# Kernel optimization log

Measured on AMD Instinct MI355X. Metric: run time of the kernel, lower is better.

Reference implementation:

```python
import jax, jax.numpy as jnp
import numpy as np

SEQ, BATCH = 2048, 32
ENC_HS, DEC_HS = 512, 1024

def setup_inputs() -> dict:
    key = jax.random.key(0)
    k1, k2, k3, k4, k5 = jax.random.split(key, 5)
    return {
        "hidden": jax.random.normal(k1, (BATCH, DEC_HS), dtype=jnp.float32),
        "encoder_outputs": jax.random.normal(k2, (SEQ, BATCH, 2 * ENC_HS), dtype=jnp.float32),
        "attn_w": jax.random.normal(k3, (2 * ENC_HS + DEC_HS, DEC_HS), dtype=jnp.float32) * 0.02,
        "attn_b": jax.random.normal(k4, (DEC_HS,), dtype=jnp.float32) * 0.02,
        "v": jax.random.normal(k5, (DEC_HS,), dtype=jnp.float32),
    }

def reference(hidden, encoder_outputs, attn_w, attn_b, v):
    # encoder_outputs: [S, B, 2*enc_hs] -> [B, S, 2*enc_hs]
    enc = jnp.transpose(encoder_outputs, (1, 0, 2))
    B, S, _ = enc.shape
    # hidden: [B, dec_hs] broadcast to [B, S, dec_hs]
    h = jnp.broadcast_to(hidden[:, None, :], (B, S, hidden.shape[-1]))
    cat = jnp.concatenate([h, enc], axis=2)            # [B, S, 2*enc_hs+dec_hs]
    energy = jnp.tanh(cat @ attn_w + attn_b)            # [B, S, dec_hs]
    scores = jnp.einsum("bsd,d->bs", energy, v)        # [B, S]
    return jax.nn.softmax(scores, axis=1)
```

## Files before the change

kernel.cpp:

```cpp
#include <hip/hip_runtime.h>


typedef _Float16 f16;
typedef _Float16 half8 __attribute__((ext_vector_type(8)));
typedef float f32x4 __attribute__((ext_vector_type(4)));

#define KDIM 1024
#define SEQ  2048
#define MROWS 65536

typedef __attribute__((address_space(1))) void gvoid;
typedef __attribute__((address_space(3))) void svoid;

__device__ __forceinline__ void gload_lds16(const void* g, void* l) {
    __builtin_amdgcn_global_load_lds((const gvoid*)g, (svoid*)l, 16, 0, 0);
}

__global__ __launch_bounds__(256) void prep_w(const float* __restrict__ w,
                                              f16* __restrict__ wt) {
    int idx  = blockIdx.x * 256 + threadIdx.x;
    int kblk = idx & 3;
    int nloc = (idx >> 2) & 255;
    int tile = idx >> 10;
    int nq   = tile >> 5, ks = tile & 31;
    int n_g  = nq * 256 + nloc;
    int kbase = 1024 + ks * 32 + kblk * 8;
    half8 h;
#pragma unroll
    for (int j = 0; j < 8; ++j)
        h[j] = (f16)w[(size_t)(kbase + j) * 1024 + n_g];
    int p = nloc * 4 + ((kblk + (nloc >> 1)) & 3);
    *(half8*)&wt[(size_t)tile * 8192 + p * 8] = h;
}

__global__ __launch_bounds__(256) void prep_hb(const float* __restrict__ hidden,
                                               const float* __restrict__ attn_w,
                                               const float* __restrict__ attn_b,
                                               float* __restrict__ hb) {
    int b = blockIdx.x >> 2;
    int n = (blockIdx.x & 3) * 256 + threadIdx.x;
    const float* h = hidden + (size_t)b * 1024;
    float acc = attn_b[n];
#pragma unroll 8
    for (int k = 0; k < 1024; ++k)
        acc += h[k] * attn_w[(size_t)k * 1024 + n];
    hb[(size_t)b * 1024 + n] = acc;
}

__global__ __launch_bounds__(512, 2)
void fused_energy(const float* __restrict__ enc, const f16* __restrict__ wt,
                  const float* __restrict__ hb, const float* __restrict__ vvec,
                  float* __restrict__ partout) {
    __shared__ f16 Ws[4][8192];
    __shared__ f16 As[4][8192];
    __shared__ float red[4][256];

    const int tid  = threadIdx.x;
    const int lane = tid & 63;
    const int wv   = tid >> 6;
    const int wm   = wv >> 2;
    const int wn   = wv & 3;
    const int l15  = lane & 15;
    const int l4   = lane >> 4;

    const int bid   = blockIdx.x;
    const int xcd   = bid & 7;
    const int chunk = bid >> 3;
    const int mt    = xcd * 32 + (chunk >> 2);
    const int nq    = chunk & 3;
    const int mrow0 = mt * 256;
    const int ncol0 = nq * 256;

    const char* wtNq = (const char*)wt + (size_t)nq * 32 * 16384;

    const int ar  = tid >> 1;
    const int akp = tid & 1;
    const float* aG = enc + (size_t)(mrow0 + ar) * KDIM + akp * 16;
    const int kb0 = akp * 2;
    const int p0  = ar * 4 + ((kb0 + (ar >> 1)) & 3);
    const int p1  = ar * 4 + ((kb0 + 1 + (ar >> 1)) & 3);

    const int wOff = wv * 2048 + lane * 16;

    char* const WsB = (char*)&Ws[0][0];
    char* const AsB = (char*)&As[0][0];

    int aOffB[8], bOffB[4];
#pragma unroll
    for (int mi = 0; mi < 8; ++mi) {
        int r = wm * 128 + mi * 16 + l15;
        aOffB[mi] = (r * 4 + ((l4 + (r >> 1)) & 3)) * 16;
    }
#pragma unroll
    for (int nj = 0; nj < 4; ++nj) {
        int n = wn * 64 + nj * 16 + l15;
        bOffB[nj] = (n * 4 + ((l4 + (n >> 1)) & 3)) * 16;
    }

    const f32x4 zero = {0.f, 0.f, 0.f, 0.f};
    f32x4 acc[8][4];
#pragma unroll
    for (int mi = 0; mi < 8; ++mi)
#pragma unroll
        for (int nj = 0; nj < 4; ++nj) acc[mi][nj] = zero;

    f32x4 aE[4], aO[4];

#define STAGE_W(TT)                                                          \
    {                                                                        \
        const char* ws_ = wtNq + (size_t)(TT) * 16384 + wOff;                \
        char* wd_ = WsB + ((TT) & 3) * 16384 + wOff;                         \
        gload_lds16(ws_, wd_);                                               \
        gload_lds16(ws_ + 1024, wd_ + 1024);                                 \
    }
#define LOAD_A(TT, R)                                                        \
    {                                                                        \
        const float* p_ = aG + (TT) * 32;                                    \
        R[0] = *(const f32x4*)(p_);     R[1] = *(const f32x4*)(p_ + 4);      \
        R[2] = *(const f32x4*)(p_ + 8); R[3] = *(const f32x4*)(p_ + 12);     \
    }
#define WRITE_A(TT, R)                                                       \
    {                                                                        \
        half8 h0_, h1_;                                                      \
        _Pragma("unroll") for (int j = 0; j < 4; ++j) {                      \
            h0_[j] = (f16)R[0][j]; h0_[4 + j] = (f16)R[1][j];                \
            h1_[j] = (f16)R[2][j]; h1_[4 + j] = (f16)R[3][j];                \
        }                                                                    \
        char* ab_ = AsB + ((TT) & 3) * 16384;                                \
        *(half8*)(ab_ + p0 * 16) = h0_;                                      \
        *(half8*)(ab_ + p1 * 16) = h1_;                                      \
    }
#define COMPUTE(TT)                                                          \
    {                                                                        \
        const char* wb_ = WsB + ((TT) & 3) * 16384;                          \
        const char* ab_ = AsB + ((TT) & 3) * 16384;                          \
        half8 bf_[4];                                                        \
        _Pragma("unroll") for (int nj = 0; nj < 4; ++nj)                     \
            bf_[nj] = *(const half8*)(wb_ + bOffB[nj]);                      \
        __builtin_amdgcn_s_setprio(1);                                       \
        _Pragma("unroll") for (int mi = 0; mi < 8; ++mi) {                   \
            half8 af_ = *(const half8*)(ab_ + aOffB[mi]);                    \
            _Pragma("unroll") for (int nj = 0; nj < 4; ++nj)                 \
                acc[mi][nj] = __builtin_amdgcn_mfma_f32_16x16x32_f16(        \
                    af_, bf_[nj], acc[mi][nj], 0, 0, 0);                     \
        }                                                                    \
        __builtin_amdgcn_s_setprio(0);                                       \
    }

    STAGE_W(0); LOAD_A(0, aE);
    STAGE_W(1); LOAD_A(1, aO);
    asm volatile("s_waitcnt vmcnt(6)" ::: "memory");
    WRITE_A(0, aE);
    asm volatile("s_waitcnt lgkmcnt(0)" ::: "memory");
    __builtin_amdgcn_s_barrier();

    for (int t = 0; t < 30; t += 2) {
        STAGE_W(t + 2); LOAD_A(t + 2, aE);
        asm volatile("s_waitcnt vmcnt(6)" ::: "memory");
        WRITE_A(t + 1, aO);
        COMPUTE(t);
        asm volatile("s_waitcnt lgkmcnt(0)" ::: "memory");
        __builtin_amdgcn_s_barrier();

        STAGE_W(t + 3); LOAD_A(t + 3, aO);
        asm volatile("s_waitcnt vmcnt(6)" ::: "memory");
        WRITE_A(t + 2, aE);
        COMPUTE(t + 1);
        asm volatile("s_waitcnt lgkmcnt(0)" ::: "memory");
        __builtin_amdgcn_s_barrier();
    }
    asm volatile("s_waitcnt vmcnt(0)" ::: "memory");
    WRITE_A(31, aO);
    COMPUTE(30);
    asm volatile("s_waitcnt lgkmcnt(0)" ::: "memory");
    __builtin_amdgcn_s_barrier();
    COMPUTE(31);

#undef STAGE_W
#undef LOAD_A
#undef WRITE_A
#undef COMPUTE

    float vv[4];
#pragma unroll
    for (int nj = 0; nj < 4; ++nj) vv[nj] = vvec[ncol0 + wn * 64 + nj * 16 + l15];
#pragma unroll
    for (int mi = 0; mi < 8; ++mi) {
#pragma unroll
        for (int rg = 0; rg < 4; ++rg) {
            int rl = wm * 128 + mi * 16 + l4 * 4 + rg;
            const float* hbrow = hb + (size_t)((mrow0 + rl) & 31) * 1024
                                 + ncol0 + wn * 64 + l15;
            float sum = 0.f;
#pragma unroll
            for (int nj = 0; nj < 4; ++nj) {
                float e  = acc[mi][nj][rg] + hbrow[nj * 16];
                float e2 = __expf(2.f * e);
                sum += (1.f - 2.f / (e2 + 1.f)) * vv[nj];
            }
            float p = sum;
            p += __shfl_xor(p, 1);
            p += __shfl_xor(p, 2);
            p += __shfl_xor(p, 4);
            p += __shfl_xor(p, 8);
            if (l15 == 0) red[wn][rl] = p;
        }
    }
    __syncthreads();
    if (tid < 256) {
        float s = red[0][tid] + red[1][tid] + red[2][tid] + red[3][tid];
        partout[(size_t)nq * MROWS + mrow0 + tid] = s;
    }
}

__global__ __launch_bounds__(256) void softmax_rows(const float* __restrict__ part,
                                                    float* __restrict__ out) {
    const int b = blockIdx.x;
    const int tid  = threadIdx.x;
    const int lane = tid & 63;
    const int wv   = tid >> 6;
    __shared__ float sred[4];
    __shared__ float ssum[4];
    float x[8];
    float mx = -3.4e38f;
#pragma unroll
    for (int j = 0; j < 8; ++j) {
        int flat = (tid + j * 256) * 32 + b;
        float v = part[flat] + part[MROWS + flat]
                + part[2 * MROWS + flat] + part[3 * MROWS + flat];
        x[j] = v;
        mx = fmaxf(mx, v);
    }
#pragma unroll
    for (int o = 1; o < 64; o <<= 1) mx = fmaxf(mx, __shfl_xor(mx, o));
    if (lane == 0) sred[wv] = mx;
    __syncthreads();
    mx = fmaxf(fmaxf(sred[0], sred[1]), fmaxf(sred[2], sred[3]));
    float s = 0.f;
#pragma unroll
    for (int j = 0; j < 8; ++j) { x[j] = __expf(x[j] - mx); s += x[j]; }
#pragma unroll
    for (int o = 1; o < 64; o <<= 1) s += __shfl_xor(s, o);
    if (lane == 0) ssum[wv] = s;
    __syncthreads();
    s = ssum[0] + ssum[1] + ssum[2] + ssum[3];
    float inv = 1.f / s;
#pragma unroll
    for (int j = 0; j < 8; ++j) out[(size_t)b * SEQ + tid + j * 256] = x[j] * inv;
}

extern "C" void kernel_launch(void* const* d_in, const int* in_sizes, int n_in,
                              void* d_out, int out_size, void* d_ws, size_t ws_size,
                              hipStream_t stream) {
    const float* hidden = (const float*)d_in[0];
    const float* enc    = (const float*)d_in[1];
    const float* attn_w = (const float*)d_in[2];
    const float* attn_b = (const float*)d_in[3];
    const float* v      = (const float*)d_in[4];
    float* out = (float*)d_out;

    f16*   wt   = (f16*)d_ws;
    float* hb   = (float*)((char*)d_ws + 2097152);
    float* part = (float*)((char*)d_ws + 2097152 + 131072);

    prep_w<<<512, 256, 0, stream>>>(attn_w, wt);
    prep_hb<<<128, 256, 0, stream>>>(hidden, attn_w, attn_b, hb);
    fused_energy<<<1024, 512, 0, stream>>>(enc, wt, hb, v, part);
    softmax_rows<<<32, 256, 0, stream>>>(part, out);
}
```

Measured before the change: 313.3 us.

## Restructure GEMM main loop into 64-wide K double-buffer with split MFMA phases

```diff
diff --git a/kernel.cpp b/kernel.cpp
--- a/kernel.cpp
+++ b/kernel.cpp
@@ -21,16 +21,16 @@
     int idx  = blockIdx.x * 256 + threadIdx.x;
     int kblk = idx & 3;
     int nloc = (idx >> 2) & 255;
-    int tile = idx >> 10;
-    int nq   = tile >> 5, ks = tile & 31;
-    int n_g  = nq * 256 + nloc;
-    int kbase = 1024 + ks * 32 + kblk * 8;
+    int tk   = idx >> 10;
+    int kk = tk & 1, tt = (tk >> 1) & 15, nq = tk >> 5;
+    int n_g = nq * 256 + nloc;
+    int kb  = 1024 + tt * 64 + kk * 32 + kblk * 8;
     half8 h;
 #pragma unroll
     for (int j = 0; j < 8; ++j)
-        h[j] = (f16)w[(size_t)(kbase + j) * 1024 + n_g];
+        h[j] = (f16)w[(size_t)(kb + j) * 1024 + n_g];
     int p = nloc * 4 + ((kblk + (nloc >> 1)) & 3);
-    *(half8*)&wt[(size_t)tile * 8192 + p * 8] = h;
+    *(half8*)&wt[(size_t)tk * 8192 + p * 8] = h;
 }
 
 __global__ __launch_bounds__(256) void prep_hb(const float* __restrict__ hidden,
@@ -51,8 +51,8 @@
 void fused_energy(const float* __restrict__ enc, const f16* __restrict__ wt,
                   const float* __restrict__ hb, const float* __restrict__ vvec,
                   float* __restrict__ partout) {
-    __shared__ f16 Ws[4][8192];
-    __shared__ f16 As[4][8192];
+    __shared__ f16 Bls[2][2][8192];
+    __shared__ f16 Als[2][2][8192];
     __shared__ float red[4][256];
 
     const int tid  = threadIdx.x;
@@ -71,19 +71,14 @@
     const int mrow0 = mt * 256;
     const int ncol0 = nq * 256;
 
-    const char* wtNq = (const char*)wt + (size_t)nq * 32 * 16384;
-
-    const int ar  = tid >> 1;
-    const int akp = tid & 1;
-    const float* aG = enc + (size_t)(mrow0 + ar) * KDIM + akp * 16;
-    const int kb0 = akp * 2;
-    const int p0  = ar * 4 + ((kb0 + (ar >> 1)) & 3);
-    const int p1  = ar * 4 + ((kb0 + 1 + (ar >> 1)) & 3);
-
-    const int wOff = wv * 2048 + lane * 16;
-
-    char* const WsB = (char*)&Ws[0][0];
-    char* const AsB = (char*)&As[0][0];
+    const char* wtNq = (const char*)wt + (size_t)nq * 16 * 2 * 16384;
+    const int stOff  = wv * 2048 + lane * 16;
+
+    const int arow = tid >> 1;
+    const int akh  = tid & 1;
+    const float* aG = enc + (size_t)(mrow0 + arow) * KDIM + akh * 16;
+    const int pw0 = arow * 4 + ((akh * 2     + (arow >> 1)) & 3);
+    const int pw1 = arow * 4 + ((akh * 2 + 1 + (arow >> 1)) & 3);
 
     int aOffB[8], bOffB[4];
 #pragma unroll
@@ -104,82 +99,130 @@
 #pragma unroll
         for (int nj = 0; nj < 4; ++nj) acc[mi][nj] = zero;
 
-    f32x4 aE[4], aO[4];
-
-#define STAGE_W(TT)                                                          \
-    {                                                                        \
-        const char* ws_ = wtNq + (size_t)(TT) * 16384 + wOff;                \
-        char* wd_ = WsB + ((TT) & 3) * 16384 + wOff;                         \
-        gload_lds16(ws_, wd_);                                               \
-        gload_lds16(ws_ + 1024, wd_ + 1024);                                 \
-    }
-#define LOAD_A(TT, R)                                                        \
-    {                                                                        \
-        const float* p_ = aG + (TT) * 32;                                    \
-        R[0] = *(const f32x4*)(p_);     R[1] = *(const f32x4*)(p_ + 4);      \
-        R[2] = *(const f32x4*)(p_ + 8); R[3] = *(const f32x4*)(p_ + 12);     \
-    }
-#define WRITE_A(TT, R)                                                       \
-    {                                                                        \
-        half8 h0_, h1_;                                                      \
-        _Pragma("unroll") for (int j = 0; j < 4; ++j) {                      \
-            h0_[j] = (f16)R[0][j]; h0_[4 + j] = (f16)R[1][j];                \
-            h1_[j] = (f16)R[2][j]; h1_[4 + j] = (f16)R[3][j];                \
-        }                                                                    \
-        char* ab_ = AsB + ((TT) & 3) * 16384;                                \
-        *(half8*)(ab_ + p0 * 16) = h0_;                                      \
-        *(half8*)(ab_ + p1 * 16) = h1_;                                      \
-    }
-#define COMPUTE(TT)                                                          \
-    {                                                                        \
-        const char* wb_ = WsB + ((TT) & 3) * 16384;                          \
-        const char* ab_ = AsB + ((TT) & 3) * 16384;                          \
-        half8 bf_[4];                                                        \
-        _Pragma("unroll") for (int nj = 0; nj < 4; ++nj)                     \
-            bf_[nj] = *(const half8*)(wb_ + bOffB[nj]);                      \
-        __builtin_amdgcn_s_setprio(1);                                       \
-        _Pragma("unroll") for (int mi = 0; mi < 8; ++mi) {                   \
-            half8 af_ = *(const half8*)(ab_ + aOffB[mi]);                    \
-            _Pragma("unroll") for (int nj = 0; nj < 4; ++nj)                 \
-                acc[mi][nj] = __builtin_amdgcn_mfma_f32_16x16x32_f16(        \
-                    af_, bf_[nj], acc[mi][nj], 0, 0, 0);                     \
-        }                                                                    \
-        __builtin_amdgcn_s_setprio(0);                                       \
-    }
-
-    STAGE_W(0); LOAD_A(0, aE);
-    STAGE_W(1); LOAD_A(1, aO);
-    asm volatile("s_waitcnt vmcnt(6)" ::: "memory");
-    WRITE_A(0, aE);
-    asm volatile("s_waitcnt lgkmcnt(0)" ::: "memory");
-    __builtin_amdgcn_s_barrier();
-
-    for (int t = 0; t < 30; t += 2) {
-        STAGE_W(t + 2); LOAD_A(t + 2, aE);
-        asm volatile("s_waitcnt vmcnt(6)" ::: "memory");
-        WRITE_A(t + 1, aO);
-        COMPUTE(t);
-        asm volatile("s_waitcnt lgkmcnt(0)" ::: "memory");
-        __builtin_amdgcn_s_barrier();
-
-        STAGE_W(t + 3); LOAD_A(t + 3, aO);
-        asm volatile("s_waitcnt vmcnt(6)" ::: "memory");
-        WRITE_A(t + 2, aE);
-        COMPUTE(t + 1);
-        asm volatile("s_waitcnt lgkmcnt(0)" ::: "memory");
-        __builtin_amdgcn_s_barrier();
-    }
-    asm volatile("s_waitcnt vmcnt(0)" ::: "memory");
-    WRITE_A(31, aO);
-    COMPUTE(30);
-    asm volatile("s_waitcnt lgkmcnt(0)" ::: "memory");
-    __builtin_amdgcn_s_barrier();
-    COMPUTE(31);
-
-#undef STAGE_W
-#undef LOAD_A
-#undef WRITE_A
-#undef COMPUTE
+    f32x4 rA0[4], rA1[4];
+    half8 bf[4], af[4];
+
+#define WAITV(N) asm volatile("s_waitcnt vmcnt(" #N ")" ::: "memory")
+#define LGKM0    asm volatile("s_waitcnt lgkmcnt(0)" ::: "memory")
+#define BAR      __builtin_amdgcn_s_barrier()
+#define PRIO1    __builtin_amdgcn_s_setprio(1)
+#define PRIO0    __builtin_amdgcn_s_setprio(0)
+
+#define STAGE_B(T, KK)                                                        \
+    {                                                                         \
+        const char* s_ = wtNq + (size_t)((T) * 2 + (KK)) * 16384 + stOff;     \
+        char* d_ = (char*)Bls + (((T) & 1) * 32768) + (KK) * 16384 + stOff;   \
+        gload_lds16(s_, d_);                                                  \
+        gload_lds16(s_ + 1024, d_ + 1024);                                    \
+    }
+#define LOADA(T, KK, R)                                                       \
+    {                                                                         \
+        const float* p_ = aG + (T) * 64 + (KK) * 32;                          \
+        R[0] = *(const f32x4*)(p_);      R[1] = *(const f32x4*)(p_ + 4);      \
+        R[2] = *(const f32x4*)(p_ + 8);  R[3] = *(const f32x4*)(p_ + 12);     \
+    }
+#define CVTA(PB, KK, R)                                                       \
+    {                                                                         \
+        half8 h0_, h1_;                                                       \
+        _Pragma("unroll") for (int j = 0; j < 4; ++j) {                       \
+            h0_[j] = (f16)R[0][j]; h0_[4 + j] = (f16)R[1][j];                 \
+            h1_[j] = (f16)R[2][j]; h1_[4 + j] = (f16)R[3][j];                 \
+        }                                                                     \
+        char* d_ = (char*)Als + (PB) * 32768 + (KK) * 16384;                  \
+        *(half8*)(d_ + pw0 * 16) = h0_;                                       \
+        *(half8*)(d_ + pw1 * 16) = h1_;                                       \
+    }
+#define READB(PC, KK)                                                         \
+    _Pragma("unroll") for (int nj = 0; nj < 4; ++nj)                          \
+        bf[nj] = *(const half8*)((char*)Bls + (PC) * 32768 + (KK) * 16384 + bOffB[nj]);
+#define READA(PC, KK, MH)                                                     \
+    _Pragma("unroll") for (int i = 0; i < 4; ++i)                             \
+        af[i] = *(const half8*)((char*)Als + (PC) * 32768 + (KK) * 16384 + aOffB[(MH) * 4 + i]);
+#define MFMA16(MH)                                                            \
+    PRIO1;                                                                    \
+    _Pragma("unroll") for (int i = 0; i < 4; ++i)                             \
+        _Pragma("unroll") for (int nj = 0; nj < 4; ++nj)                      \
+            acc[(MH) * 4 + i][nj] = __builtin_amdgcn_mfma_f32_16x16x32_f16(   \
+                af[i], bf[nj], acc[(MH) * 4 + i][nj], 0, 0, 0);               \
+    PRIO0;
+
+    STAGE_B(0, 0); STAGE_B(0, 1);
+    LOADA(0, 0, rA0); LOADA(0, 1, rA1);
+    WAITV(4);
+    CVTA(0, 0, rA0);
+    WAITV(0);
+    CVTA(0, 1, rA1);
+    LOADA(1, 0, rA0); LOADA(1, 1, rA1);
+    LGKM0; BAR;
+
+    for (int t = 0; t < 14; ++t) {
+        const int cur = t & 1, nxt = cur ^ 1;
+        STAGE_B(t + 1, 0);
+        WAITV(10);
+        READB(cur, 0); READA(cur, 0, 0);
+        MFMA16(0);
+        BAR;
+        STAGE_B(t + 1, 1);
+        READA(cur, 0, 1);
+        MFMA16(1);
+        BAR;
+        WAITV(8);
+        CVTA(nxt, 0, rA0);
+        LOADA(t + 2, 0, rA0);
+        READB(cur, 1); READA(cur, 1, 0);
+        MFMA16(0);
+        LGKM0; BAR;
+        WAITV(2);
+        CVTA(nxt, 1, rA1);
+        LOADA(t + 2, 1, rA1);
+        READA(cur, 1, 1);
+        MFMA16(1);
+        LGKM0; BAR;
+    }
+    {
+        const int cur = 0, nxt = 1;
+        STAGE_B(15, 0);
+        WAITV(10);
+        READB(cur, 0); READA(cur, 0, 0);
+        MFMA16(0);
+        BAR;
+        STAGE_B(15, 1);
+        READA(cur, 0, 1);
+        MFMA16(1);
+        BAR;
+        WAITV(8);
+        CVTA(nxt, 0, rA0);
+        READB(cur, 1); READA(cur, 1, 0);
+        MFMA16(0);
+        LGKM0; BAR;
+        WAITV(2);
+        CVTA(nxt, 1, rA1);
+        READA(cur, 1, 1);
+        MFMA16(1);
+        LGKM0; BAR;
+    }
+    {
+        const int cur = 1;
+        WAITV(0);
+        READB(cur, 0); READA(cur, 0, 0);
+        MFMA16(0);
+        BAR;
+        READA(cur, 0, 1);
+        MFMA16(1);
+        BAR;
+        READB(cur, 1); READA(cur, 1, 0);
+        MFMA16(0);
+        BAR;
+        READA(cur, 1, 1);
+        MFMA16(1);
+    }
+
+#undef STAGE_B
+#undef LOADA
+#undef CVTA
+#undef READB
+#undef READA
+#undef MFMA16
 
     float vv[4];
 #pragma unroll
```

New measurement: 291.9 us. 1.07x faster.

## Load A fragments directly into registers and deepen B LDS pipeline to 8 stages

Applied to the files above, without the earlier changes.

```diff
diff --git a/kernel.cpp b/kernel.cpp
--- a/kernel.cpp
+++ b/kernel.cpp
@@ -21,16 +21,16 @@
     int idx  = blockIdx.x * 256 + threadIdx.x;
     int kblk = idx & 3;
     int nloc = (idx >> 2) & 255;
-    int tile = idx >> 10;
-    int nq   = tile >> 5, ks = tile & 31;
+    int tk   = idx >> 10;
+    int ks   = tk & 31, nq = tk >> 5;
     int n_g  = nq * 256 + nloc;
-    int kbase = 1024 + ks * 32 + kblk * 8;
+    int kb   = 1024 + ks * 32 + kblk * 8;
     half8 h;
 #pragma unroll
     for (int j = 0; j < 8; ++j)
-        h[j] = (f16)w[(size_t)(kbase + j) * 1024 + n_g];
+        h[j] = (f16)w[(size_t)(kb + j) * 1024 + n_g];
     int p = nloc * 4 + ((kblk + (nloc >> 1)) & 3);
-    *(half8*)&wt[(size_t)tile * 8192 + p * 8] = h;
+    *(half8*)&wt[(size_t)tk * 8192 + p * 8] = h;
 }
 
 __global__ __launch_bounds__(256) void prep_hb(const float* __restrict__ hidden,
@@ -51,15 +51,14 @@
 void fused_energy(const float* __restrict__ enc, const f16* __restrict__ wt,
                   const float* __restrict__ hb, const float* __restrict__ vvec,
                   float* __restrict__ partout) {
-    __shared__ f16 Ws[4][8192];
-    __shared__ f16 As[4][8192];
-    __shared__ float red[4][256];
+    __shared__ f16 Bls[8][8192];
+    __shared__ float red[2][256];
 
     const int tid  = threadIdx.x;
     const int lane = tid & 63;
     const int wv   = tid >> 6;
-    const int wm   = wv >> 2;
-    const int wn   = wv & 3;
+    const int wm   = wv >> 1;
+    const int wn   = wv & 1;
     const int l15  = lane & 15;
     const int l4   = lane >> 4;
 
@@ -73,127 +72,108 @@
 
     const char* wtNq = (const char*)wt + (size_t)nq * 32 * 16384;
 
-    const int ar  = tid >> 1;
-    const int akp = tid & 1;
-    const float* aG = enc + (size_t)(mrow0 + ar) * KDIM + akp * 16;
-    const int kb0 = akp * 2;
-    const int p0  = ar * 4 + ((kb0 + (ar >> 1)) & 3);
-    const int p1  = ar * 4 + ((kb0 + 1 + (ar >> 1)) & 3);
-
-    const int wOff = wv * 2048 + lane * 16;
-
-    char* const WsB = (char*)&Ws[0][0];
-    char* const AsB = (char*)&As[0][0];
-
-    int aOffB[8], bOffB[4];
-#pragma unroll
-    for (int mi = 0; mi < 8; ++mi) {
-        int r = wm * 128 + mi * 16 + l15;
-        aOffB[mi] = (r * 4 + ((l4 + (r >> 1)) & 3)) * 16;
-    }
-#pragma unroll
-    for (int nj = 0; nj < 4; ++nj) {
-        int n = wn * 64 + nj * 16 + l15;
+    const float* aB0 = enc + (size_t)(mrow0 + wm * 64 +  0 + l15) * KDIM + l4 * 8;
+    const float* aB1 = enc + (size_t)(mrow0 + wm * 64 + 16 + l15) * KDIM + l4 * 8;
+    const float* aB2 = enc + (size_t)(mrow0 + wm * 64 + 32 + l15) * KDIM + l4 * 8;
+    const float* aB3 = enc + (size_t)(mrow0 + wm * 64 + 48 + l15) * KDIM + l4 * 8;
+
+    int bOffB[8];
+#pragma unroll
+    for (int nj = 0; nj < 8; ++nj) {
+        int n = wn * 128 + nj * 16 + l15;
         bOffB[nj] = (n * 4 + ((l4 + (n >> 1)) & 3)) * 16;
     }
 
     const f32x4 zero = {0.f, 0.f, 0.f, 0.f};
-    f32x4 acc[8][4];
-#pragma unroll
-    for (int mi = 0; mi < 8; ++mi)
-#pragma unroll
-        for (int nj = 0; nj < 4; ++nj) acc[mi][nj] = zero;
-
-    f32x4 aE[4], aO[4];
-
-#define STAGE_W(TT)                                                          \
-    {                                                                        \
-        const char* ws_ = wtNq + (size_t)(TT) * 16384 + wOff;                \
-        char* wd_ = WsB + ((TT) & 3) * 16384 + wOff;                         \
-        gload_lds16(ws_, wd_);                                               \
-        gload_lds16(ws_ + 1024, wd_ + 1024);                                 \
-    }
-#define LOAD_A(TT, R)                                                        \
-    {                                                                        \
-        const float* p_ = aG + (TT) * 32;                                    \
-        R[0] = *(const f32x4*)(p_);     R[1] = *(const f32x4*)(p_ + 4);      \
-        R[2] = *(const f32x4*)(p_ + 8); R[3] = *(const f32x4*)(p_ + 12);     \
-    }
-#define WRITE_A(TT, R)                                                       \
-    {                                                                        \
-        half8 h0_, h1_;                                                      \
-        _Pragma("unroll") for (int j = 0; j < 4; ++j) {                      \
-            h0_[j] = (f16)R[0][j]; h0_[4 + j] = (f16)R[1][j];                \
-            h1_[j] = (f16)R[2][j]; h1_[4 + j] = (f16)R[3][j];                \
-        }                                                                    \
-        char* ab_ = AsB + ((TT) & 3) * 16384;                                \
-        *(half8*)(ab_ + p0 * 16) = h0_;                                      \
-        *(half8*)(ab_ + p1 * 16) = h1_;                                      \
-    }
-#define COMPUTE(TT)                                                          \
-    {                                                                        \
-        const char* wb_ = WsB + ((TT) & 3) * 16384;                          \
-        const char* ab_ = AsB + ((TT) & 3) * 16384;                          \
-        half8 bf_[4];                                                        \
-        _Pragma("unroll") for (int nj = 0; nj < 4; ++nj)                     \
-            bf_[nj] = *(const half8*)(wb_ + bOffB[nj]);                      \
-        __builtin_amdgcn_s_setprio(1);                                       \
-        _Pragma("unroll") for (int mi = 0; mi < 8; ++mi) {                   \
-            half8 af_ = *(const half8*)(ab_ + aOffB[mi]);                    \
-            _Pragma("unroll") for (int nj = 0; nj < 4; ++nj)                 \
-                acc[mi][nj] = __builtin_amdgcn_mfma_f32_16x16x32_f16(        \
-                    af_, bf_[nj], acc[mi][nj], 0, 0, 0);                     \
-        }                                                                    \
-        __builtin_amdgcn_s_setprio(0);                                       \
-    }
-
-    STAGE_W(0); LOAD_A(0, aE);
-    STAGE_W(1); LOAD_A(1, aO);
-    asm volatile("s_waitcnt vmcnt(6)" ::: "memory");
-    WRITE_A(0, aE);
-    asm volatile("s_waitcnt lgkmcnt(0)" ::: "memory");
-    __builtin_amdgcn_s_barrier();
-
-    for (int t = 0; t < 30; t += 2) {
-        STAGE_W(t + 2); LOAD_A(t + 2, aE);
-        asm volatile("s_waitcnt vmcnt(6)" ::: "memory");
-        WRITE_A(t + 1, aO);
-        COMPUTE(t);
-        asm volatile("s_waitcnt lgkmcnt(0)" ::: "memory");
-        __builtin_amdgcn_s_barrier();
-
-        STAGE_W(t + 3); LOAD_A(t + 3, aO);
-        asm volatile("s_waitcnt vmcnt(6)" ::: "memory");
-        WRITE_A(t + 2, aE);
-        COMPUTE(t + 1);
-        asm volatile("s_waitcnt lgkmcnt(0)" ::: "memory");
-        __builtin_amdgcn_s_barrier();
-    }
-    asm volatile("s_waitcnt vmcnt(0)" ::: "memory");
-    WRITE_A(31, aO);
-    COMPUTE(30);
-    asm volatile("s_waitcnt lgkmcnt(0)" ::: "memory");
-    __builtin_amdgcn_s_barrier();
-    COMPUTE(31);
-
-#undef STAGE_W
-#undef LOAD_A
-#undef WRITE_A
+    f32x4 acc[4][8];
+#pragma unroll
+    for (int mi = 0; mi < 4; ++mi)
+#pragma unroll
+        for (int nj = 0; nj < 8; ++nj) acc[mi][nj] = zero;
+
+    f32x4 rAa[8], rAb[8];
+    half8 af[4];
+
+#define WAITV(N) asm volatile("s_waitcnt vmcnt(" #N ")" ::: "memory")
+#define BAR      __builtin_amdgcn_s_barrier()
+#define PRIO1    __builtin_amdgcn_s_setprio(1)
+#define PRIO0    __builtin_amdgcn_s_setprio(0)
+
+#define STAGE_B(J)                                                            \
+    {                                                                         \
+        const char* s_ = wtNq + (size_t)(J) * 16384 + tid * 16;               \
+        char* d_ = (char*)&Bls[(J) & 7][0] + tid * 16;                        \
+        gload_lds16(s_, d_);                                                  \
+        gload_lds16(s_ + 8192, d_ + 8192);                                    \
+    }
+#define LOADA(J, R)                                                           \
+    {                                                                         \
+        R[0] = *(const f32x4*)(aB0 + (J) * 32); R[1] = *(const f32x4*)(aB0 + (J) * 32 + 4); \
+        R[2] = *(const f32x4*)(aB1 + (J) * 32); R[3] = *(const f32x4*)(aB1 + (J) * 32 + 4); \
+        R[4] = *(const f32x4*)(aB2 + (J) * 32); R[5] = *(const f32x4*)(aB2 + (J) * 32 + 4); \
+        R[6] = *(const f32x4*)(aB3 + (J) * 32); R[7] = *(const f32x4*)(aB3 + (J) * 32 + 4); \
+    }
+#define CVTA(R)                                                               \
+    _Pragma("unroll") for (int mi = 0; mi < 4; ++mi)                          \
+        _Pragma("unroll") for (int j = 0; j < 4; ++j) {                       \
+            af[mi][j]     = (f16)R[2 * mi][j];                                \
+            af[mi][4 + j] = (f16)R[2 * mi + 1][j];                            \
+        }
+#define COMPUTE(J)                                                            \
+    {                                                                         \
+        const char* bb_ = (const char*)&Bls[(J) & 7][0];                      \
+        PRIO1;                                                                \
+        _Pragma("unroll") for (int nj = 0; nj < 8; ++nj) {                    \
+            half8 bf_ = *(const half8*)(bb_ + bOffB[nj]);                     \
+            _Pragma("unroll") for (int mi = 0; mi < 4; ++mi)                  \
+                acc[mi][nj] = __builtin_amdgcn_mfma_f32_16x16x32_f16(         \
+                    af[mi], bf_, acc[mi][nj], 0, 0, 0);                       \
+        }                                                                     \
+        PRIO0;                                                                \
+    }
+#define STEP(J, CONS, LOAD)                                                   \
+    {                                                                         \
+        BAR;                                                                  \
+        LOADA((J) + 1, LOAD);                                                 \
+        STAGE_B((J) + 4);                                                     \
+        WAITV(10);                                                            \
+        CVTA(CONS);                                                           \
+        COMPUTE(J);                                                           \
+    }
+
+    STAGE_B(0); STAGE_B(1); STAGE_B(2); STAGE_B(3);
+    LOADA(0, rAa);
+    WAITV(0);
+
+    for (int j = 0; j < 28; j += 2) {
+        STEP(j,     rAa, rAb);
+        STEP(j + 1, rAb, rAa);
+    }
+    BAR; LOADA(29, rAb); WAITV(8); CVTA(rAa); COMPUTE(28);
+    BAR; LOADA(30, rAa); WAITV(8); CVTA(rAb); COMPUTE(29);
+    BAR; LOADA(31, rAb); WAITV(8); CVTA(rAa); COMPUTE(30);
+    BAR;                 WAITV(0); CVTA(rAb); COMPUTE(31);
+
+#undef STAGE_B
+#undef LOADA
+#undef CVTA
 #undef COMPUTE
-
-    float vv[4];
-#pragma unroll
-    for (int nj = 0; nj < 4; ++nj) vv[nj] = vvec[ncol0 + wn * 64 + nj * 16 + l15];
-#pragma unroll
-    for (int mi = 0; mi < 8; ++mi) {
+#undef STEP
+
+    float vv[8];
+#pragma unroll
+    for (int nj = 0; nj < 8; ++nj)
+        vv[nj] = vvec[ncol0 + wn * 128 + nj * 16 + l15];
+#pragma unroll
+    for (int mi = 0; mi < 4; ++mi) {
 #pragma unroll
         for (int rg = 0; rg < 4; ++rg) {
-            int rl = wm * 128 + mi * 16 + l4 * 4 + rg;
+            int rl = wm * 64 + mi * 16 + l4 * 4 + rg;
             const float* hbrow = hb + (size_t)((mrow0 + rl) & 31) * 1024
-                                 + ncol0 + wn * 64 + l15;
+                                 + ncol0 + wn * 128 + l15;
             float sum = 0.f;
 #pragma unroll
-            for (int nj = 0; nj < 4; ++nj) {
+            for (int nj = 0; nj < 8; ++nj) {
                 float e  = acc[mi][nj][rg] + hbrow[nj * 16];
                 float e2 = __expf(2.f * e);
                 sum += (1.f - 2.f / (e2 + 1.f)) * vv[nj];
@@ -208,7 +188,7 @@
     }
     __syncthreads();
     if (tid < 256) {
-        float s = red[0][tid] + red[1][tid] + red[2][tid] + red[3][tid];
+        float s = red[0][tid] + red[1][tid];
         partout[(size_t)nq * MROWS + mrow0 + tid] = s;
     }
 }
```

Result: slower. 403.9 us (+28.9%).
